# Performance work log

Measured on AMD Instinct MI355X. Metric: run time of the kernel, lower is better.

The kernel has to match this reference:

```python
import jax, jax.numpy as jnp
import numpy as np
import math

BASE_RES = 16
MAX_RES = 2048
LEVELS = 16
FEAT_DIM = 2
LOG_B = math.log(MAX_RES / BASE_RES) / (LEVELS - 1)  # per-level log scale


def setup_inputs() -> dict:
    key = jax.random.key(0)
    k1, k2 = jax.random.split(key)
    B = 1048576
    positions = jax.random.uniform(k1, (B, 3), dtype=jnp.float32)
    total = MAX_RES * MAX_RES * 3 * FEAT_DIM
    # torch.nn.init.uniform_ -> U[0,1)
    plane_table = jax.random.uniform(k2, (total,), dtype=jnp.float32)
    return {"positions": positions, "plane_table": plane_table}


def _encode(positions, plane_table):
    B = positions.shape[0]
    dtype = positions.dtype
    # planes: (xy, yz, zx) -> [B, 3 planes, 2 coords]
    x, y, z = positions[:, 0], positions[:, 1], positions[:, 2]
    xyz6 = jnp.stack([x, y, y, z, z, x], axis=1).reshape(B, 3, 2)
    planes = plane_table.reshape(3, MAX_RES * MAX_RES, FEAT_DIM)
    plane_ids = jnp.arange(3)  # [3]
    outs = []
    for level in range(LEVELS):
        scale = BASE_RES * math.exp(level * LOG_B) - 1.0
        res = int(math.ceil(scale)) + 1  # grid_resolution
        pos = xyz6 * (res - 1) + 0.5            # [B,3,2]
        pg = jnp.floor(pos)
        frac = pos - pg                          # fractional part
        pg = pg.astype(jnp.int32)
        local = jnp.zeros((B, 3, FEAT_DIM), dtype)
        for idx in range(4):  # 4 bilinear corners
            w = jnp.ones((B, 3), dtype)
            coords = []
            for d in range(2):
                if idx & (1 << d):
                    coords.append(pg[..., d] + 1)
                    w = w * frac[..., d]
                else:
                    coords.append(pg[..., d])
                    w = w * (1.0 - frac[..., d])
            c = jnp.stack(coords, axis=-1).astype(dtype)  # [B,3,2]
            # remap corner from level grid to the max_res storage grid (truncating cast)
            c_ori = (c / res * (MAX_RES - 1)).astype(jnp.int32)
            index = c_ori[..., 0] + c_ori[..., 1] * MAX_RES  # [B,3] flat plane index
            feats = planes[plane_ids[None, :], index]        # [B,3,FEAT_DIM] gather
            local = local + w[..., None] * feats
        # cross-plane product
        outs.append(local[:, 0] * local[:, 1] * local[:, 2])  # [B,FEAT_DIM]
    out = jnp.stack(outs, axis=2)  # [B, FEAT_DIM, LEVELS]; sn = j*LEVELS + level
    return out.reshape(B, FEAT_DIM * LEVELS)


def reference(positions, plane_table):
    return _encode(positions, plane_table)
```

## Files before the change

### kernel.cpp

```cpp
#include <hip/hip_runtime.h>
#include <math.h>

#define LEVELS 16
#define MAX_RES 2048
#define NCELL_BITS 5
#define NCELLS (1 << (3 * NCELL_BITS))
#define LC_LO 9
#define LC_HI 12
#define NLC (LC_HI - LC_LO + 1)

typedef float nfloat4 __attribute__((ext_vector_type(4)));
typedef float nfloat2 __attribute__((ext_vector_type(2)));

struct ResParams {
  int res[LEVELS];
  int coff[LEVELS];
  int S[LEVELS];
  int bstart[NLC + 1];
};


__device__ __forceinline__ unsigned int morton5(int cx, int cy, int cz) {
  unsigned int k = 0;
  #pragma unroll
  for (int b = 0; b < NCELL_BITS; ++b)
    k |= (((cx >> b) & 1) << (3 * b)) | (((cy >> b) & 1) << (3 * b + 1)) |
         (((cz >> b) & 1) << (3 * b + 2));
  return k;
}

__device__ __forceinline__ unsigned int cell_of(float x, float y, float z) {
  int cx = min(31, max(0, (int)(x * 32.0f)));
  int cy = min(31, max(0, (int)(y * 32.0f)));
  int cz = min(31, max(0, (int)(z * 32.0f)));
  return morton5(cx, cy, cz);
}

__global__ __launch_bounds__(256) void build_and_hist(
    const float* __restrict__ table, float2* __restrict__ compact,
    const float* __restrict__ pos, unsigned int* __restrict__ hist,
    ResParams P, int B, int nbuild)
{
  __shared__ nfloat2 rowbuf[MAX_RES];
  int b = blockIdx.x;

  if (b < nbuild) {
    int li = 0;
    #pragma unroll
    for (int k = 1; k < NLC; ++k) if (b >= P.bstart[k]) li = k;
    int l = LC_LO + li;
    int res = P.res[l];
    int W = res + 1;
    int rem = b - P.bstart[li];
    int p = rem / W;
    int v = rem - p * W;
    const float fres = (float)res;

    int cv = (int)(__fmul_rn(__fdiv_rn((float)v, fres), 2047.0f));
    const float* src = table + (size_t)p * (MAX_RES * MAX_RES * 2) + (size_t)(cv << 11) * 2;

    const nfloat4* src4 = reinterpret_cast<const nfloat4*>(src);
    #pragma unroll
    for (int j = (int)threadIdx.x; j < MAX_RES / 2; j += 256) {
      nfloat4 r = src4[j];
      rowbuf[j * 2]     = nfloat2{r.x, r.y};
      rowbuf[j * 2 + 1] = nfloat2{r.z, r.w};
    }
    __syncthreads();

    float2* dst = compact + (P.coff[l] + p * P.S[l] + v * W);
    for (int u = (int)threadIdx.x; u < W; u += 256) {
      int cu = (int)(__fmul_rn(__fdiv_rn((float)u, fres), 2047.0f));
      nfloat2 e = rowbuf[cu];
      dst[u] = make_float2(e.x, e.y);
    }
  } else {
    int i = (b - nbuild) * 256 + (int)threadIdx.x;
    if (i < B)
      atomicAdd(&hist[cell_of(pos[i*3], pos[i*3+1], pos[i*3+2])], 1u);
  }
}

__global__ __launch_bounds__(256) void scan_partial(const unsigned int* __restrict__ hist,
                                                    unsigned int* __restrict__ offs,
                                                    unsigned int* __restrict__ partials) {
  __shared__ unsigned int sh[256];
  int tid = (int)threadIdx.x;
  int c = blockIdx.x * 256 + tid;
  unsigned int v = hist[c];
  sh[tid] = v;
  __syncthreads();
  #pragma unroll
  for (int off = 1; off < 256; off <<= 1) {
    unsigned int u = (tid >= off) ? sh[tid - off] : 0u;
    __syncthreads();
    sh[tid] += u;
    __syncthreads();
  }
  offs[c] = sh[tid] - v;
  if (tid == 255) partials[blockIdx.x] = sh[255];
}

__global__ __launch_bounds__(128) void scan_roots(unsigned int* __restrict__ partials,
                                                  unsigned int* __restrict__ roots) {
  __shared__ unsigned int sh[128];
  int tid = (int)threadIdx.x;
  unsigned int v = partials[tid];
  sh[tid] = v;
  __syncthreads();
  #pragma unroll
  for (int off = 1; off < 128; off <<= 1) {
    unsigned int u = (tid >= off) ? sh[tid - off] : 0u;
    __syncthreads();
    sh[tid] += u;
    __syncthreads();
  }
  roots[tid] = sh[tid] - v;
}

__global__ __launch_bounds__(256) void scatter_kernel(const float* __restrict__ pos,
                                                      unsigned int* __restrict__ offs,
                                                      const unsigned int* __restrict__ roots,
                                                      nfloat4* __restrict__ sorted, int B) {
  int i = blockIdx.x * 256 + (int)threadIdx.x;
  if (i >= B) return;
  float x = pos[i*3], y = pos[i*3+1], z = pos[i*3+2];
  unsigned int k = cell_of(x, y, z);
  unsigned int slot = roots[k >> 8] + atomicAdd(&offs[k], 1u);
  nfloat4 v = {x, y, z, __int_as_float(i)};
  sorted[slot] = v;
}


template <bool USE_COMPACT>
__global__ __launch_bounds__(256) void triplane_main(
    const nfloat4* __restrict__ sorted,
    const float* __restrict__ table,
    const float2* __restrict__ compact,
    float* __restrict__ out,
    ResParams P, int B, int nwg)
{
  int wg = blockIdx.x;
  int q = nwg >> 3, r = nwg & 7;
  int xcd = wg & 7, idx = wg >> 3;
  int swz = (xcd < r) ? xcd * (q + 1) + idx : r * (q + 1) + (xcd - r) * q + idx;
  int t = swz * 256 + (int)threadIdx.x;
  if (t >= B) return;

  nfloat4 s = sorted[t];
  float x = s.x, y = s.y, z = s.z;
  int orig = __float_as_int(s.w);

  float uarr[3] = {x, y, z};
  float varr[3] = {y, z, x};

  float o0[LEVELS], o1[LEVELS];

  #pragma unroll
  for (int l = 0; l < LEVELS; ++l) {
    const int   res   = P.res[l];
    const float resm1 = (float)(res - 1);
    const float fres  = (float)res;
    const bool  cpath = USE_COMPACT && (l >= LC_LO && l <= LC_HI);

    float prod0 = 1.0f, prod1 = 1.0f;

    #pragma unroll
    for (int p = 0; p < 3; ++p) {
      float pu = __fadd_rn(__fmul_rn(uarr[p], resm1), 0.5f);
      float pv = __fadd_rn(__fmul_rn(varr[p], resm1), 0.5f);
      float gu = floorf(pu), gv = floorf(pv);
      float fu = __fsub_rn(pu, gu);
      float fv = __fsub_rn(pv, gv);

      float f00x, f00y, f10x, f10y, f01x, f01y, f11x, f11y;

      if (cpath) {
        int iu = (int)gu, iv = (int)gv;
        int W = res + 1;
        const float2* lv = compact + (P.coff[l] + p * P.S[l]);
        int i0 = iv * W + iu;
        const nfloat4 r0 = *reinterpret_cast<const nfloat4*>(lv + i0);
        const nfloat4 r1 = *reinterpret_cast<const nfloat4*>(lv + i0 + W);
        f00x = r0.x; f00y = r0.y; f10x = r0.z; f10y = r0.w;
        f01x = r1.x; f01y = r1.y; f11x = r1.z; f11y = r1.w;
      } else {
        float gu1 = __fadd_rn(gu, 1.0f);
        float gv1 = __fadd_rn(gv, 1.0f);
        int cou0 = (int)(__fmul_rn(__fdiv_rn(gu,  fres), 2047.0f));
        int cou1 = (int)(__fmul_rn(__fdiv_rn(gu1, fres), 2047.0f));
        int cov0 = (int)(__fmul_rn(__fdiv_rn(gv,  fres), 2047.0f));
        int cov1 = (int)(__fmul_rn(__fdiv_rn(gv1, fres), 2047.0f));

        const float* plane = table + (size_t)p * (MAX_RES * MAX_RES * 2);

        if (l == 15) {
          const nfloat4 r0 = *reinterpret_cast<const nfloat4*>(plane + (size_t)(cou0 + (cov0 << 11)) * 2);
          const nfloat4 r1 = *reinterpret_cast<const nfloat4*>(plane + (size_t)(cou0 + (cov1 << 11)) * 2);
          const bool adj = (cou1 != cou0);
          f00x = r0.x; f00y = r0.y;
          f10x = adj ? r0.z : r0.x;  f10y = adj ? r0.w : r0.y;
          f01x = r1.x; f01y = r1.y;
          f11x = adj ? r1.z : r1.x;  f11y = adj ? r1.w : r1.y;
        } else {
          const float2 f00 = *reinterpret_cast<const float2*>(plane + (size_t)(cou0 + (cov0 << 11)) * 2);
          const float2 f10 = *reinterpret_cast<const float2*>(plane + (size_t)(cou1 + (cov0 << 11)) * 2);
          const float2 f01 = *reinterpret_cast<const float2*>(plane + (size_t)(cou0 + (cov1 << 11)) * 2);
          const float2 f11 = *reinterpret_cast<const float2*>(plane + (size_t)(cou1 + (cov1 << 11)) * 2);
          f00x = f00.x; f00y = f00.y; f10x = f10.x; f10y = f10.y;
          f01x = f01.x; f01y = f01.y; f11x = f11.x; f11y = f11.y;
        }
      }

      float w00 = (1.0f - fu) * (1.0f - fv);
      float w10 = fu * (1.0f - fv);
      float w01 = (1.0f - fu) * fv;
      float w11 = fu * fv;

      float a0 = 0.0f, a1 = 0.0f;
      a0 += w00 * f00x;  a1 += w00 * f00y;
      a0 += w10 * f10x;  a1 += w10 * f10y;
      a0 += w01 * f01x;  a1 += w01 * f01y;
      a0 += w11 * f11x;  a1 += w11 * f11y;

      prod0 *= a0;
      prod1 *= a1;
    }

    o0[l] = prod0;
    o1[l] = prod1;
  }

  nfloat4* base = reinterpret_cast<nfloat4*>(out + (size_t)orig * 32);
  #pragma unroll
  for (int k = 0; k < 4; ++k) {
    nfloat4 v0 = {o0[k*4+0], o0[k*4+1], o0[k*4+2], o0[k*4+3]};
    nfloat4 v1 = {o1[k*4+0], o1[k*4+1], o1[k*4+2], o1[k*4+3]};
    base[k] = v0;
    base[4 + k] = v1;
  }
}

extern "C" void kernel_launch(void* const* d_in, const int* in_sizes, int n_in,
                              void* d_out, int out_size, void* d_ws, size_t ws_size,
                              hipStream_t stream) {
  const float* positions = (const float*)d_in[0];
  const float* table     = (const float*)d_in[1];
  float* out             = (float*)d_out;
  int B = in_sizes[0] / 3;

  ResParams P;
  const double LOG_B = log(2048.0 / 16.0) / (double)(LEVELS - 1);
  int runoff = 0;
  for (int l = 0; l < LEVELS; ++l) {
    double scale = 16.0 * exp((double)l * LOG_B) - 1.0;
    P.res[l] = (int)ceil(scale) + 1;
    P.coff[l] = 0; P.S[l] = 0;
  }
  int nbuild = 0;
  for (int li = 0; li < NLC; ++li) {
    int l = LC_LO + li;
    int W = P.res[l] + 1;
    P.S[l] = W * W;
    P.coff[l] = runoff;
    runoff += 3 * P.S[l];
    P.bstart[li] = nbuild;
    nbuild += 3 * W;
  }
  P.bstart[NLC] = nbuild;

  int nwg = (B + 255) / 256;

  size_t off_hist    = 0;
  size_t off_offs    = off_hist + (size_t)NCELLS * 4;
  size_t off_part    = off_offs + (size_t)NCELLS * 4;
  size_t off_roots   = off_part + 128 * 4;
  size_t off_sorted  = ((off_roots + 128 * 4) + 255) & ~(size_t)255;
  size_t off_compact = off_sorted + (size_t)B * 16;
  size_t need_sort   = off_compact;
  size_t need_all    = off_compact + (size_t)runoff * 8;

  if (ws_size < need_sort) return;

  unsigned int* hist  = (unsigned int*)((char*)d_ws + off_hist);
  unsigned int* offs  = (unsigned int*)((char*)d_ws + off_offs);
  unsigned int* part  = (unsigned int*)((char*)d_ws + off_part);
  unsigned int* roots = (unsigned int*)((char*)d_ws + off_roots);
  nfloat4*      srt   = (nfloat4*)((char*)d_ws + off_sorted);
  float2*       cmp   = (float2*)((char*)d_ws + off_compact);

  const bool use_compact = (ws_size >= need_all);
  const int nb = use_compact ? nbuild : 0;

  hipMemsetAsync(hist, 0, (size_t)NCELLS * 4, stream);
  hipLaunchKernelGGL(build_and_hist, dim3(nb + nwg), dim3(256), 0, stream,
                     table, cmp, positions, hist, P, B, nb);
  hipLaunchKernelGGL(scan_partial, dim3(NCELLS / 256), dim3(256), 0, stream, hist, offs, part);
  hipLaunchKernelGGL(scan_roots, dim3(1), dim3(128), 0, stream, part, roots);
  hipLaunchKernelGGL(scatter_kernel, dim3(nwg), dim3(256), 0, stream,
                     positions, offs, roots, srt, B);

  if (use_compact) {
    hipLaunchKernelGGL((triplane_main<true>), dim3(nwg), dim3(256), 0, stream,
                       srt, table, cmp, out, P, B, nwg);
  } else {
    hipLaunchKernelGGL((triplane_main<false>), dim3(nwg), dim3(256), 0, stream,
                       srt, table, cmp, out, P, B, nwg);
  }
}
```

Baseline: 451.6 us.

## Fuse root scan into scatter and store index permutation instead of sorted positions

Removes the single-block scan_roots launch by having every scatter block redo the 128-entry prefix scan in shared memory. Scatter now writes only a 4-byte original index per slot instead of a 16-byte float4 holding position and index. The main kernel then gathers positions through the permutation, which trades a smaller sequential write for scattered 12-byte reads from the positions array. It also saves one kernel launch and cuts the size of the workspace.

```diff
diff --git a/kernel.cpp b/kernel.cpp
--- a/kernel.cpp
+++ b/kernel.cpp
@@ -101,40 +101,35 @@
   if (tid == 255) partials[blockIdx.x] = sh[255];
 }
 
-__global__ __launch_bounds__(128) void scan_roots(unsigned int* __restrict__ partials,
-                                                  unsigned int* __restrict__ roots) {
-  __shared__ unsigned int sh[128];
+__global__ __launch_bounds__(256) void scatter_perm(const float* __restrict__ pos,
+                                                    unsigned int* __restrict__ offs,
+                                                    const unsigned int* __restrict__ partials,
+                                                    unsigned int* __restrict__ perm, int B) {
+  __shared__ unsigned int rsh[128];
   int tid = (int)threadIdx.x;
-  unsigned int v = partials[tid];
-  sh[tid] = v;
+  if (tid < 128) rsh[tid] = partials[tid];
   __syncthreads();
   #pragma unroll
   for (int off = 1; off < 128; off <<= 1) {
-    unsigned int u = (tid >= off) ? sh[tid - off] : 0u;
-    __syncthreads();
-    sh[tid] += u;
-    __syncthreads();
-  }
-  roots[tid] = sh[tid] - v;
-}
-
-__global__ __launch_bounds__(256) void scatter_kernel(const float* __restrict__ pos,
-                                                      unsigned int* __restrict__ offs,
-                                                      const unsigned int* __restrict__ roots,
-                                                      nfloat4* __restrict__ sorted, int B) {
-  int i = blockIdx.x * 256 + (int)threadIdx.x;
+    unsigned int u = (tid < 128 && tid >= off) ? rsh[tid - off] : 0u;
+    __syncthreads();
+    if (tid < 128) rsh[tid] += u;
+    __syncthreads();
+  }
+  int i = blockIdx.x * 256 + tid;
   if (i >= B) return;
   float x = pos[i*3], y = pos[i*3+1], z = pos[i*3+2];
   unsigned int k = cell_of(x, y, z);
-  unsigned int slot = roots[k >> 8] + atomicAdd(&offs[k], 1u);
-  nfloat4 v = {x, y, z, __int_as_float(i)};
-  sorted[slot] = v;
-}
-
+  unsigned int seg = k >> 8;
+  unsigned int root = rsh[seg] - partials[seg];
+  unsigned int slot = root + atomicAdd(&offs[k], 1u);
+  perm[slot] = (unsigned int)i;
+}
 
 template <bool USE_COMPACT>
 __global__ __launch_bounds__(256) void triplane_main(
-    const nfloat4* __restrict__ sorted,
+    const unsigned int* __restrict__ perm,
+    const float* __restrict__ positions,
     const float* __restrict__ table,
     const float2* __restrict__ compact,
     float* __restrict__ out,
@@ -147,9 +142,10 @@
   int t = swz * 256 + (int)threadIdx.x;
   if (t >= B) return;
 
-  nfloat4 s = sorted[t];
-  float x = s.x, y = s.y, z = s.z;
-  int orig = __float_as_int(s.w);
+  int orig = (int)perm[t];
+  float x = positions[(size_t)orig * 3 + 0];
+  float y = positions[(size_t)orig * 3 + 1];
+  float z = positions[(size_t)orig * 3 + 2];
 
   float uarr[3] = {x, y, z};
   float varr[3] = {y, z, x};
@@ -274,9 +270,8 @@
   size_t off_hist    = 0;
   size_t off_offs    = off_hist + (size_t)NCELLS * 4;
   size_t off_part    = off_offs + (size_t)NCELLS * 4;
-  size_t off_roots   = off_part + 128 * 4;
-  size_t off_sorted  = ((off_roots + 128 * 4) + 255) & ~(size_t)255;
-  size_t off_compact = off_sorted + (size_t)B * 16;
+  size_t off_perm    = ((off_part + 128 * 4) + 255) & ~(size_t)255;
+  size_t off_compact = off_perm + (size_t)B * 4;
   size_t need_sort   = off_compact;
   size_t need_all    = off_compact + (size_t)runoff * 8;
 
@@ -285,8 +280,7 @@
   unsigned int* hist  = (unsigned int*)((char*)d_ws + off_hist);
   unsigned int* offs  = (unsigned int*)((char*)d_ws + off_offs);
   unsigned int* part  = (unsigned int*)((char*)d_ws + off_part);
-  unsigned int* roots = (unsigned int*)((char*)d_ws + off_roots);
-  nfloat4*      srt   = (nfloat4*)((char*)d_ws + off_sorted);
+  unsigned int* perm  = (unsigned int*)((char*)d_ws + off_perm);
   float2*       cmp   = (float2*)((char*)d_ws + off_compact);
 
   const bool use_compact = (ws_size >= need_all);
@@ -296,15 +290,14 @@
   hipLaunchKernelGGL(build_and_hist, dim3(nb + nwg), dim3(256), 0, stream,
                      table, cmp, positions, hist, P, B, nb);
   hipLaunchKernelGGL(scan_partial, dim3(NCELLS / 256), dim3(256), 0, stream, hist, offs, part);
-  hipLaunchKernelGGL(scan_roots, dim3(1), dim3(128), 0, stream, part, roots);
-  hipLaunchKernelGGL(scatter_kernel, dim3(nwg), dim3(256), 0, stream,
-                     positions, offs, roots, srt, B);
+  hipLaunchKernelGGL(scatter_perm, dim3(nwg), dim3(256), 0, stream,
+                     positions, offs, part, perm, B);
 
   if (use_compact) {
     hipLaunchKernelGGL((triplane_main<true>), dim3(nwg), dim3(256), 0, stream,
-                       srt, table, cmp, out, P, B, nwg);
+                       perm, positions, table, cmp, out, P, B, nwg);
   } else {
     hipLaunchKernelGGL((triplane_main<false>), dim3(nwg), dim3(256), 0, stream,
-                       srt, table, cmp, out, P, B, nwg);
-  }
-}
+                       perm, positions, table, cmp, out, P, B, nwg);
+  }
+}
```

Result: no change. 454.9 us (+0.7%).
